# Kernel tuning notes

Measured on AMD Instinct MI355X. Metric: run time of the kernel, lower is better.

## Reference

```python
import jax, jax.numpy as jnp
import numpy as np
import math

D_MODEL = 1024
D_ATTN = 128
D_MID = 128
L = 4096

def setup_inputs() -> dict:
    key = jax.random.key(0)
    ks = jax.random.split(key, 5)
    scale = 1.0 / math.sqrt(D_MODEL)
    return {
        "x": jax.random.normal(ks[0], (L, D_MODEL), jnp.float32),
        "z": jax.random.normal(ks[1], (L, D_MODEL), jnp.float32),
        "Wq": jax.random.normal(ks[2], (D_MODEL, D_ATTN), jnp.float32) * scale,
        "bq": jnp.zeros((D_ATTN,), jnp.float32),
        "Wk": jax.random.normal(ks[3], (D_MODEL, D_ATTN), jnp.float32) * scale,
        "bk": jnp.zeros((D_ATTN,), jnp.float32),
        "Wv": jax.random.normal(ks[4], (D_MODEL, D_MID), jnp.float32) * scale,
        "bv": jnp.zeros((D_MID,), jnp.float32),
    }

def reference(x, z, Wq, bq, Wk, bk, Wv, bv):
    # q: [L_x, d_attn], k: [L_z, d_attn], v: [L_z, d_mid]
    q = x @ Wq + bq
    k = z @ Wk + bk
    v = z @ Wv + bv
    inv_sqrt_d = 1.0 / math.sqrt(D_ATTN)
    s = (q @ k.T) * inv_sqrt_d            # [L_x, L_z]
    y = jax.nn.softmax(s, axis=-1) @ v    # [L_x, d_mid]
    return y
```

## Files before the change

kernel.cpp:

```cpp
#include <hip/hip_runtime.h>
#include <hip/hip_bf16.h>

typedef __attribute__((ext_vector_type(8))) short short8;
typedef __attribute__((ext_vector_type(4))) float f32x4;

#define L_SEQ 4096
#define DM    1024
#define DA    128
#define AZ    8

#define OFF_QB  786432
#define OFF_KF  1835008
#define OFF_VF  2883584
#define OFF_OA  4063232

__device__ __forceinline__ short f2bf(float f) {
    union { float f; unsigned u; } v; v.f = f;
    unsigned u = v.u;
    u += 0x7FFFu + ((u >> 16) & 1u);
    return (short)(u >> 16);
}

typedef const __attribute__((address_space(1))) void g_void_t;
typedef __attribute__((address_space(3))) void l_void_t;
__device__ __forceinline__ void g2lds16(const void* g, void* l) {
    __builtin_amdgcn_global_load_lds((g_void_t*)g, (l_void_t*)l, 16, 0, 0);
}

__global__ __launch_bounds__(256) void prep_w_kernel(
    const float* __restrict__ Wq, const float* __restrict__ Wk,
    const float* __restrict__ Wv, short8* __restrict__ WTf)
{
    const int m = blockIdx.y, kidx = blockIdx.x;
    const float* __restrict__ W = (m == 0) ? Wq : (m == 1) ? Wk : Wv;
    __shared__ __align__(16) float Ws[32 * 132];
    const int t = threadIdx.x;
#pragma unroll
    for (int i = 0; i < 4; i++) {
        const int u = i * 256 + t;
        const int kk = u >> 5, n4 = (u & 31) * 4;
        *(f32x4*)&Ws[kk * 132 + n4] = *(const f32x4*)&W[(size_t)(kidx * 32 + kk) * DA + n4];
    }
    __syncthreads();
#pragma unroll
    for (int i = 0; i < 2; i++) {
        const int u = i * 256 + t;
        const int nt = u >> 6, lane = u & 63, l16 = lane & 15, quad = lane >> 4;
        short8 fr;
#pragma unroll
        for (int j = 0; j < 8; j++)
            fr[j] = f2bf(Ws[(quad * 8 + j) * 132 + nt * 16 + l16]);
        WTf[((size_t)(m * 32 + kidx) * 8 + nt) * 64 + lane] = fr;
    }
}

__global__ __launch_bounds__(256, 1) void qkv_kernel(
    const float* __restrict__ x, const float* __restrict__ z,
    const char* __restrict__ WTraw,
    const float* __restrict__ bq, const float* __restrict__ bk,
    const float* __restrict__ bv,
    short* __restrict__ qb, short8* __restrict__ kf, short8* __restrict__ vf)
{
    __shared__ __align__(16) char smem[2][32768];

    const int t = threadIdx.x;
    const int wave = t >> 6, lane = t & 63;
    const int l16 = lane & 15, quad = lane >> 4;
    const int mtile = wave >> 1, nhalf = wave & 1;
    const int isKV = blockIdx.y;
    const int m1 = isKV ? 1 : 0;
    const int row0 = blockIdx.x * 32;
    const int nbytes = isKV ? 32768 : 16384;

    const float* __restrict__ Am = isKV ? z : x;
    const float* ap = Am + (size_t)(row0 + mtile * 16 + l16) * DM + quad * 8;

    f32x4 acc1[4], acc2[4];
#pragma unroll
    for (int i = 0; i < 4; i++) {
        acc1[i] = (f32x4){0.f, 0.f, 0.f, 0.f};
        acc2[i] = (f32x4){0.f, 0.f, 0.f, 0.f};
    }

    auto stage = [&](int it2, int b) {
        const char* base1 = WTraw + (size_t)(m1 * 32 + it2 * 2) * 8192;
        const char* base2 = WTraw + (size_t)(2 * 32 + it2 * 2) * 8192;
#pragma unroll
        for (int i = 0; i < 8; i++) {
            const int off = i * 4096 + wave * 1024;
            if (off < nbytes) {
                const char* src = (off < 16384) ? (base1 + off) : (base2 + (off - 16384));
                g2lds16(src + lane * 16, &smem[b][off]);
            }
        }
    };

    f32x4 cur[4], nxt[4];
#pragma unroll
    for (int j = 0; j < 2; j++) {
        cur[j * 2]     = *(const f32x4*)(ap + j * 32);
        cur[j * 2 + 1] = *(const f32x4*)(ap + j * 32 + 4);
        nxt[j * 2]     = *(const f32x4*)(ap + 64 + j * 32);
        nxt[j * 2 + 1] = *(const f32x4*)(ap + 64 + j * 32 + 4);
    }

    stage(0, 0);
    __syncthreads();

#pragma unroll 1
    for (int it = 0; it < 16; it++) {
        const int b = it & 1;
        if (it + 1 < 16) stage(it + 1, b ^ 1);

        const int ipf = (it + 2 < 16) ? it + 2 : it;
        f32x4 fut[4];
#pragma unroll
        for (int j = 0; j < 2; j++) {
            fut[j * 2]     = *(const f32x4*)(ap + ipf * 64 + j * 32);
            fut[j * 2 + 1] = *(const f32x4*)(ap + ipf * 64 + j * 32 + 4);
        }

#pragma unroll
        for (int ss = 0; ss < 2; ss++) {
            short8 afr;
#pragma unroll
            for (int j = 0; j < 4; j++) {
                afr[j]     = f2bf(cur[ss * 2][j]);
                afr[4 + j] = f2bf(cur[ss * 2 + 1][j]);
            }
#pragma unroll
            for (int ntl = 0; ntl < 4; ntl++) {
                short8 bfr = *(const short8*)&smem[b][ss * 8192 + ((nhalf * 4 + ntl) * 64 + lane) * 16];
                acc1[ntl] = __builtin_amdgcn_mfma_f32_16x16x32_bf16(afr, bfr, acc1[ntl], 0, 0, 0);
            }
            if (isKV) {
#pragma unroll
                for (int ntl = 0; ntl < 4; ntl++) {
                    short8 bfr = *(const short8*)&smem[b][16384 + ss * 8192 + ((nhalf * 4 + ntl) * 64 + lane) * 16];
                    acc2[ntl] = __builtin_amdgcn_mfma_f32_16x16x32_bf16(afr, bfr, acc2[ntl], 0, 0, 0);
                }
            }
        }
        __syncthreads();
#pragma unroll
        for (int j = 0; j < 4; j++) { cur[j] = nxt[j]; nxt[j] = fut[j]; }
    }

    if (!isKV) {
#pragma unroll
        for (int ntl = 0; ntl < 4; ntl++) {
            const int col = nhalf * 64 + ntl * 16 + l16;
            const float bb = bq[col];
#pragma unroll
            for (int r = 0; r < 4; r++)
                qb[(size_t)(row0 + mtile * 16 + quad * 4 + r) * DA + col] =
                    f2bf(acc1[ntl][r] + bb);
        }
        return;
    }

    short* kT = (short*)&smem[0][0];
    short* vT = (short*)&smem[0][16384];
#pragma unroll
    for (int ntl = 0; ntl < 4; ntl++) {
        const int col = nhalf * 64 + ntl * 16 + l16;
        const float bbk = bk[col], bbv = bv[col];
#pragma unroll
        for (int r = 0; r < 4; r++) {
            const int rl = mtile * 16 + quad * 4 + r;
            kT[rl * 132 + col] = f2bf(acc1[ntl][r] + bbk);
            vT[rl * 132 + col] = f2bf(acc2[ntl][r] + bbv);
        }
    }
    __syncthreads();

    const int kg = blockIdx.x;
#pragma unroll
    for (int i = 0; i < 2; i++) {
        const int f = i * 256 + t;
        const int ks = f >> 7, nth = (f >> 6) & 1, ln = f & 63;
        const int lf = ln & 15, qf = ln >> 4;
        short8 fr;
#pragma unroll
        for (int j = 0; j < 8; j++)
            fr[j] = kT[(nth * 16 + lf) * 132 + ks * 32 + qf * 8 + j];
        kf[((size_t)(kg * 4 + ks) * 2 + nth) * 64 + ln] = fr;
    }
#pragma unroll
    for (int i = 0; i < 3; i++) {
        const int f = i * 256 + t;
        if (f < 576) {
            const int nt = f >> 6, ln = f & 63;
            const int lf = ln & 15, qf = ln >> 4;
            short8 fr;
            if (nt < 8) {
#pragma unroll
                for (int j = 0; j < 8; j++)
                    fr[j] = vT[(qf * 8 + j) * 132 + nt * 16 + lf];
            } else {
                const short one = (short)0x3F80;
#pragma unroll
                for (int j = 0; j < 8; j++) fr[j] = (lf == 0) ? one : (short)0;
            }
            vf[((size_t)kg * 9 + nt) * 64 + ln] = fr;
        }
    }
}

__global__ __launch_bounds__(256, 2) void attn_kernel(
    const short* __restrict__ qb, const char* __restrict__ kfg,
    const char* __restrict__ vfg, float* __restrict__ OA,
    float* __restrict__ lA)
{
    __shared__ __align__(16) char kv[2][17408];
    __shared__ __align__(16) short Ps[4][16 * 40];

    const int t    = threadIdx.x;
    const int wave = t >> 6;
    const int lane = t & 63;
    const int l16  = lane & 15;
    const int quad = lane >> 4;
    const int qr0  = blockIdx.x * 64;
    const int g0   = blockIdx.y * 16;

    auto stage = [&](int g, int b) {
        const char* kb_ = kfg + (size_t)(g0 + g) * 8192;
        const char* vb_ = vfg + (size_t)(g0 + g) * 9216;
#pragma unroll
        for (int i = 0; i < 5; i++) {
            const int off = i * 4096 + wave * 1024;
            if (off < 17408) {
                const char* src = (off < 8192) ? (kb_ + off) : (vb_ + (off - 8192));
                g2lds16(src + lane * 16, &kv[b][off]);
            }
        }
    };

    stage(0, 0);

    short8 af[4];
    const short* qrow = qb + (size_t)(qr0 + wave * 16 + l16) * DA + quad * 8;
#pragma unroll
    for (int ks = 0; ks < 4; ks++)
        af[ks] = *(const short8*)(qrow + ks * 32);

    f32x4 O[9];
#pragma unroll
    for (int i = 0; i < 9; i++) O[i] = (f32x4){0.f, 0.f, 0.f, 0.f};

    const float C = 0.08838834764831845f;
    short* P = &Ps[wave][0];

    __syncthreads();

#pragma unroll 1
    for (int g = 0; g < 16; g++) {
        const int b = g & 1;
        if (g + 1 < 16) stage(g + 1, b ^ 1);

        const char* kb_ = &kv[b][0];
        const char* vb_ = &kv[b][8192];

        f32x4 s0[2];
#pragma unroll
        for (int nh = 0; nh < 2; nh++) s0[nh] = (f32x4){0.f, 0.f, 0.f, 0.f};
#pragma unroll
        for (int nh = 0; nh < 2; nh++)
#pragma unroll
            for (int ks = 0; ks < 4; ks++) {
                short8 bfr = *(const short8*)(kb_ + ((ks * 2 + nh) * 64 + lane) * 16);
                s0[nh] = __builtin_amdgcn_mfma_f32_16x16x32_bf16(af[ks], bfr, s0[nh], 0, 0, 0);
            }

#pragma unroll
        for (int nh = 0; nh < 2; nh++)
#pragma unroll
            for (int r = 0; r < 4; r++)
                P[(quad * 4 + r) * 40 + nh * 16 + l16] = f2bf(__expf(s0[nh][r] * C));
        asm volatile("" ::: "memory");
        __builtin_amdgcn_s_waitcnt(0xc07f);
        asm volatile("" ::: "memory");

        short8 a2 = *(const short8*)&P[l16 * 40 + quad * 8];
#pragma unroll
        for (int nt = 0; nt < 9; nt++) {
            short8 b2 = *(const short8*)(vb_ + (nt * 64 + lane) * 16);
            O[nt] = __builtin_amdgcn_mfma_f32_16x16x32_bf16(a2, b2, O[nt], 0, 0, 0);
        }
        __syncthreads();
    }

    const int rw = qr0 + wave * 16;
    float* Ob = OA + (size_t)blockIdx.y * L_SEQ * DA;
#pragma unroll
    for (int nt = 0; nt < 8; nt++)
#pragma unroll
        for (int r = 0; r < 4; r++)
            Ob[(size_t)(rw + quad * 4 + r) * DA + nt * 16 + l16] = O[nt][r];
    if (l16 == 0) {
        float* lb = lA + (size_t)blockIdx.y * L_SEQ;
#pragma unroll
        for (int r = 0; r < 4; r++)
            lb[rw + quad * 4 + r] = O[8][r];
    }
}

__global__ __launch_bounds__(256) void merge_kernel(
    const float* __restrict__ OA, const float* __restrict__ lA,
    float* __restrict__ out)
{
    const int t = threadIdx.x;
    const int row = blockIdx.x * 16 + (t >> 4);
    const int cg = (t & 15) * 8;

    f32x4 a0 = (f32x4){0.f, 0.f, 0.f, 0.f};
    f32x4 a1 = (f32x4){0.f, 0.f, 0.f, 0.f};
    float lsum = 0.f;
#pragma unroll
    for (int zz = 0; zz < AZ; zz++) {
        const float* p = &OA[((size_t)zz * L_SEQ + row) * DA + cg];
        a0 = a0 + *(const f32x4*)p;
        a1 = a1 + *(const f32x4*)(p + 4);
        lsum += lA[(size_t)zz * L_SEQ + row];
    }
    const float inv = 1.f / lsum;
    f32x4* dst = (f32x4*)&out[(size_t)row * DA + cg];
    dst[0] = a0 * inv;
    dst[1] = a1 * inv;
}

extern "C" void kernel_launch(void* const* d_in, const int* in_sizes, int n_in,
                              void* d_out, int out_size, void* d_ws, size_t ws_size,
                              hipStream_t stream) {
    (void)in_sizes; (void)n_in; (void)out_size; (void)ws_size;
    const float* x  = (const float*)d_in[0];
    const float* z  = (const float*)d_in[1];
    const float* Wq = (const float*)d_in[2];
    const float* bq = (const float*)d_in[3];
    const float* Wk = (const float*)d_in[4];
    const float* bk = (const float*)d_in[5];
    const float* Wv = (const float*)d_in[6];
    const float* bv = (const float*)d_in[7];
    float* out = (float*)d_out;

    short8* WTf = (short8*)d_ws;
    short*  qb  = (short*)((char*)d_ws + OFF_QB);
    short8* kf  = (short8*)((char*)d_ws + OFF_KF);
    short8* vf  = (short8*)((char*)d_ws + OFF_VF);
    float*  OA  = (float*)((char*)d_ws + OFF_OA);
    float*  lA  = (float*)((char*)d_ws + OFF_OA + (size_t)AZ * L_SEQ * DA * 4);

    prep_w_kernel<<<dim3(32, 3), 256, 0, stream>>>(Wq, Wk, Wv, WTf);
    qkv_kernel<<<dim3(128, 2), 256, 0, stream>>>(x, z, (const char*)WTf,
                                                 bq, bk, bv, qb, kf, vf);
    attn_kernel<<<dim3(64, AZ), 256, 0, stream>>>(qb, (const char*)kf,
                                                  (const char*)vf, OA, lA);
    merge_kernel<<<256, 256, 0, stream>>>(OA, lA, out);
}
```

Baseline: 129.9 us.

## Give each attention wave two query tiles, fold scale into Q, and drop ones-column from V

```diff
diff --git a/kernel.cpp b/kernel.cpp
--- a/kernel.cpp
+++ b/kernel.cpp
@@ -19,6 +19,12 @@
     unsigned u = v.u;
     u += 0x7FFFu + ((u >> 16) & 1u);
     return (short)(u >> 16);
+}
+
+__device__ __forceinline__ unsigned cvt_pk_bf16(float lo, float hi) {
+    unsigned r;
+    asm("v_cvt_pk_bf16_f32 %0, %1, %2" : "=v"(r) : "v"(lo), "v"(hi));
+    return r;
 }
 
 typedef const __attribute__((address_space(1))) void g_void_t;
@@ -147,6 +153,7 @@
     }
 
     if (!isKV) {
+        const float CL2E = 0.1275187669712930f;
 #pragma unroll
         for (int ntl = 0; ntl < 4; ntl++) {
             const int col = nhalf * 64 + ntl * 16 + l16;
@@ -154,7 +161,7 @@
 #pragma unroll
             for (int r = 0; r < 4; r++)
                 qb[(size_t)(row0 + mtile * 16 + quad * 4 + r) * DA + col] =
-                    f2bf(acc1[ntl][r] + bb);
+                    f2bf((acc1[ntl][r] + bb) * CL2E);
         }
         return;
     }
@@ -187,33 +194,25 @@
         kf[((size_t)(kg * 4 + ks) * 2 + nth) * 64 + ln] = fr;
     }
 #pragma unroll
-    for (int i = 0; i < 3; i++) {
+    for (int i = 0; i < 2; i++) {
         const int f = i * 256 + t;
-        if (f < 576) {
-            const int nt = f >> 6, ln = f & 63;
-            const int lf = ln & 15, qf = ln >> 4;
-            short8 fr;
-            if (nt < 8) {
-#pragma unroll
-                for (int j = 0; j < 8; j++)
-                    fr[j] = vT[(qf * 8 + j) * 132 + nt * 16 + lf];
-            } else {
-                const short one = (short)0x3F80;
-#pragma unroll
-                for (int j = 0; j < 8; j++) fr[j] = (lf == 0) ? one : (short)0;
-            }
-            vf[((size_t)kg * 9 + nt) * 64 + ln] = fr;
-        }
-    }
-}
-
-__global__ __launch_bounds__(256, 2) void attn_kernel(
+        const int nt = f >> 6, ln = f & 63;
+        const int lf = ln & 15, qf = ln >> 4;
+        short8 fr;
+#pragma unroll
+        for (int j = 0; j < 8; j++)
+            fr[j] = vT[(qf * 8 + j) * 132 + nt * 16 + lf];
+        vf[((size_t)kg * 8 + nt) * 64 + ln] = fr;
+    }
+}
+
+__global__ __launch_bounds__(128, 1) void attn_kernel(
     const short* __restrict__ qb, const char* __restrict__ kfg,
     const char* __restrict__ vfg, float* __restrict__ OA,
     float* __restrict__ lA)
 {
-    __shared__ __align__(16) char kv[2][17408];
-    __shared__ __align__(16) short Ps[4][16 * 40];
+    __shared__ __align__(16) char kv[2][16384];
+    __shared__ __align__(16) short Ps[2][32 * 40];
 
     const int t    = threadIdx.x;
     const int wave = t >> 6;
@@ -225,30 +224,36 @@
 
     auto stage = [&](int g, int b) {
         const char* kb_ = kfg + (size_t)(g0 + g) * 8192;
-        const char* vb_ = vfg + (size_t)(g0 + g) * 9216;
-#pragma unroll
-        for (int i = 0; i < 5; i++) {
-            const int off = i * 4096 + wave * 1024;
-            if (off < 17408) {
-                const char* src = (off < 8192) ? (kb_ + off) : (vb_ + (off - 8192));
-                g2lds16(src + lane * 16, &kv[b][off]);
-            }
+        const char* vb_ = vfg + (size_t)(g0 + g) * 8192;
+#pragma unroll
+        for (int i = 0; i < 8; i++) {
+            const int off = i * 2048 + wave * 1024;
+            const char* src = (off < 8192) ? (kb_ + off) : (vb_ + (off - 8192));
+            g2lds16(src + lane * 16, &kv[b][off]);
         }
     };
 
     stage(0, 0);
 
-    short8 af[4];
-    const short* qrow = qb + (size_t)(qr0 + wave * 16 + l16) * DA + quad * 8;
-#pragma unroll
-    for (int ks = 0; ks < 4; ks++)
-        af[ks] = *(const short8*)(qrow + ks * 32);
-
-    f32x4 O[9];
-#pragma unroll
-    for (int i = 0; i < 9; i++) O[i] = (f32x4){0.f, 0.f, 0.f, 0.f};
-
-    const float C = 0.08838834764831845f;
+    short8 af[2][4];
+#pragma unroll
+    for (int mt = 0; mt < 2; mt++) {
+        const short* qrow = qb + (size_t)(qr0 + wave * 32 + mt * 16 + l16) * DA + quad * 8;
+#pragma unroll
+        for (int ks = 0; ks < 4; ks++)
+            af[mt][ks] = *(const short8*)(qrow + ks * 32);
+    }
+
+    short8 bones;
+#pragma unroll
+    for (int j = 0; j < 8; j++) bones[j] = (l16 == 0) ? (short)0x3F80 : (short)0;
+
+    f32x4 O[2][9];
+#pragma unroll
+    for (int mt = 0; mt < 2; mt++)
+#pragma unroll
+        for (int i = 0; i < 9; i++) O[mt][i] = (f32x4){0.f, 0.f, 0.f, 0.f};
+
     short* P = &Ps[wave][0];
 
     __syncthreads();
@@ -261,47 +266,71 @@
         const char* kb_ = &kv[b][0];
         const char* vb_ = &kv[b][8192];
 
-        f32x4 s0[2];
-#pragma unroll
-        for (int nh = 0; nh < 2; nh++) s0[nh] = (f32x4){0.f, 0.f, 0.f, 0.f};
-#pragma unroll
-        for (int nh = 0; nh < 2; nh++)
-#pragma unroll
-            for (int ks = 0; ks < 4; ks++) {
-                short8 bfr = *(const short8*)(kb_ + ((ks * 2 + nh) * 64 + lane) * 16);
-                s0[nh] = __builtin_amdgcn_mfma_f32_16x16x32_bf16(af[ks], bfr, s0[nh], 0, 0, 0);
-            }
-
-#pragma unroll
-        for (int nh = 0; nh < 2; nh++)
-#pragma unroll
-            for (int r = 0; r < 4; r++)
-                P[(quad * 4 + r) * 40 + nh * 16 + l16] = f2bf(__expf(s0[nh][r] * C));
+        f32x4 s0[2][2];
+#pragma unroll
+        for (int mt = 0; mt < 2; mt++)
+#pragma unroll
+            for (int nh = 0; nh < 2; nh++) s0[mt][nh] = (f32x4){0.f, 0.f, 0.f, 0.f};
+#pragma unroll
+        for (int ks = 0; ks < 4; ks++)
+#pragma unroll
+            for (int nh = 0; nh < 2; nh++) {
+                const short8 bfr = *(const short8*)(kb_ + ((ks * 2 + nh) * 64 + lane) * 16);
+                s0[0][nh] = __builtin_amdgcn_mfma_f32_16x16x32_bf16(af[0][ks], bfr, s0[0][nh], 0, 0, 0);
+                s0[1][nh] = __builtin_amdgcn_mfma_f32_16x16x32_bf16(af[1][ks], bfr, s0[1][nh], 0, 0, 0);
+            }
+
+        short8 b2v[8];
+#pragma unroll
+        for (int nt = 0; nt < 8; nt++)
+            b2v[nt] = *(const short8*)(vb_ + (nt * 64 + lane) * 16);
+
+#pragma unroll
+        for (int mt = 0; mt < 2; mt++)
+#pragma unroll
+            for (int nh = 0; nh < 2; nh++)
+#pragma unroll
+                for (int rp = 0; rp < 2; rp++) {
+                    const float e0 = exp2f(s0[mt][nh][rp * 2]);
+                    const float e1 = exp2f(s0[mt][nh][rp * 2 + 1]);
+                    const unsigned pk = cvt_pk_bf16(e0, e1);
+                    const int row = mt * 16 + quad * 4 + rp * 2;
+                    P[row * 40 + nh * 16 + l16]       = (short)(pk & 0xffff);
+                    P[(row + 1) * 40 + nh * 16 + l16] = (short)(pk >> 16);
+                }
         asm volatile("" ::: "memory");
         __builtin_amdgcn_s_waitcnt(0xc07f);
         asm volatile("" ::: "memory");
 
-        short8 a2 = *(const short8*)&P[l16 * 40 + quad * 8];
-#pragma unroll
-        for (int nt = 0; nt < 9; nt++) {
-            short8 b2 = *(const short8*)(vb_ + (nt * 64 + lane) * 16);
-            O[nt] = __builtin_amdgcn_mfma_f32_16x16x32_bf16(a2, b2, O[nt], 0, 0, 0);
-        }
+        short8 a2[2];
+        a2[0] = *(const short8*)&P[l16 * 40 + quad * 8];
+        a2[1] = *(const short8*)&P[(16 + l16) * 40 + quad * 8];
+#pragma unroll
+        for (int nt = 0; nt < 8; nt++) {
+            O[0][nt] = __builtin_amdgcn_mfma_f32_16x16x32_bf16(a2[0], b2v[nt], O[0][nt], 0, 0, 0);
+            O[1][nt] = __builtin_amdgcn_mfma_f32_16x16x32_bf16(a2[1], b2v[nt], O[1][nt], 0, 0, 0);
+        }
+        O[0][8] = __builtin_amdgcn_mfma_f32_16x16x32_bf16(a2[0], bones, O[0][8], 0, 0, 0);
+        O[1][8] = __builtin_amdgcn_mfma_f32_16x16x32_bf16(a2[1], bones, O[1][8], 0, 0, 0);
         __syncthreads();
     }
 
-    const int rw = qr0 + wave * 16;
+    const int rw = qr0 + wave * 32;
     float* Ob = OA + (size_t)blockIdx.y * L_SEQ * DA;
 #pragma unroll
-    for (int nt = 0; nt < 8; nt++)
-#pragma unroll
-        for (int r = 0; r < 4; r++)
-            Ob[(size_t)(rw + quad * 4 + r) * DA + nt * 16 + l16] = O[nt][r];
+    for (int mt = 0; mt < 2; mt++)
+#pragma unroll
+        for (int nt = 0; nt < 8; nt++)
+#pragma unroll
+            for (int r = 0; r < 4; r++)
+                Ob[(size_t)(rw + mt * 16 + quad * 4 + r) * DA + nt * 16 + l16] = O[mt][nt][r];
     if (l16 == 0) {
         float* lb = lA + (size_t)blockIdx.y * L_SEQ;
 #pragma unroll
-        for (int r = 0; r < 4; r++)
-            lb[rw + quad * 4 + r] = O[8][r];
+        for (int mt = 0; mt < 2; mt++)
+#pragma unroll
+            for (int r = 0; r < 4; r++)
+                lb[rw + mt * 16 + quad * 4 + r] = O[mt][8][r];
     }
 }
 
@@ -353,7 +382,7 @@
     prep_w_kernel<<<dim3(32, 3), 256, 0, stream>>>(Wq, Wk, Wv, WTf);
     qkv_kernel<<<dim3(128, 2), 256, 0, stream>>>(x, z, (const char*)WTf,
                                                  bq, bk, bv, qb, kf, vf);
-    attn_kernel<<<dim3(64, AZ), 256, 0, stream>>>(qb, (const char*)kf,
+    attn_kernel<<<dim3(64, AZ), 128, 0, stream>>>(qb, (const char*)kf,
                                                   (const char*)vf, OA, lA);
     merge_kernel<<<256, 256, 0, stream>>>(OA, lA, out);
 }
```

Measured after the change: 137.0 us. 5.5% more time.
